# Kernel optimization log

Measured on AMD Instinct MI355X. Metric: run time of the kernel, lower is better.

Reference implementation:

```python
import jax, jax.numpy as jnp
import numpy as np

NUM_GRAPHS = 16
NODES_PER_GRAPH = 2048
FEAT_DIM = 512


def setup_inputs() -> dict:
    key = jax.random.key(0)
    batched_h = jax.random.normal(key, (NUM_GRAPHS * NODES_PER_GRAPH, FEAT_DIM), dtype=jnp.float32)
    return {
        "batched_h": batched_h,
        "num_graphs": NUM_GRAPHS,
        "nodes_per_graph": NODES_PER_GRAPH,
    }


def reference(batched_h, num_graphs, nodes_per_graph):
    # Wq = Wk = Identity (module defaults), return_feat = False.
    # Per graph g: sm[i, j] = sum_d (q[i, d] - k[j, d])^2
    # computed via the Gram-matrix identity ||q||^2 + ||k||^2 - 2 q k^T,
    # which replaces the original O(n^2 * d) tiled intermediate with a GEMM.
    h = batched_h.reshape(num_graphs, nodes_per_graph, -1)  # [G, N, D]
    q = h
    k = h
    sq_q = jnp.sum(q * q, axis=-1)                      # [G, N]
    sq_k = jnp.sum(k * k, axis=-1)                      # [G, N]
    gram = jnp.einsum("gnd,gmd->gnm", q, k)             # [G, N, N]
    sm = sq_q[:, :, None] + sq_k[:, None, :] - 2.0 * gram
    return sm  # [G, N, N] stacked analogue of the per-graph inst_out list
```

## Files before the change

### kernel.cpp

```cpp
#include <hip/hip_runtime.h>
#include <hip/hip_bf16.h>
#include <stdint.h>

#define NG 16
#define NN 2048
#define DD 512
#define NROW (NG * NN)
#define NTILE 16
#define NPAIR 136
#define NXCD 8

typedef __attribute__((ext_vector_type(8))) short short8;
typedef __attribute__((ext_vector_type(4))) float f32x4;

__device__ inline unsigned short f2bf(float f) {
  union { float f; unsigned int u; } c;
  c.f = f;
  unsigned int x = c.u;
  unsigned int r = (x + 0x7fffu + ((x >> 16) & 1u)) >> 16;
  return (unsigned short)r;
}

__device__ inline void gload_lds16(const void* g, void* l) {
  __builtin_amdgcn_global_load_lds(
      (const __attribute__((address_space(1))) void*)g,
      (__attribute__((address_space(3))) void*)l, 16, 0, 0);
}

__device__ inline void barrier_lds_only() {
  asm volatile("s_waitcnt lgkmcnt(0)" ::: "memory");
  __builtin_amdgcn_s_barrier();
}

template <bool WRITE_BF>
__global__ __launch_bounds__(256) void prep_kernel(const float* __restrict__ h,
                                                   unsigned short* __restrict__ hbf,
                                                   float* __restrict__ sq) {
  const int row = blockIdx.x * 4 + (threadIdx.x >> 6);
  const int lane = threadIdx.x & 63;
  const float* hr = h + (size_t)row * DD;
  float4 v0 = ((const float4*)hr)[lane * 2];
  float4 v1 = ((const float4*)hr)[lane * 2 + 1];
  float s = v0.x * v0.x + v0.y * v0.y + v0.z * v0.z + v0.w * v0.w +
            v1.x * v1.x + v1.y * v1.y + v1.z * v1.z + v1.w * v1.w;
  if (WRITE_BF) {
    union { unsigned short us[8]; uint4 u4; } pk;
    pk.us[0] = f2bf(v0.x); pk.us[1] = f2bf(v0.y);
    pk.us[2] = f2bf(v0.z); pk.us[3] = f2bf(v0.w);
    pk.us[4] = f2bf(v1.x); pk.us[5] = f2bf(v1.y);
    pk.us[6] = f2bf(v1.z); pk.us[7] = f2bf(v1.w);
    ((uint4*)(hbf + (size_t)row * DD))[lane] = pk.u4;
  }
#pragma unroll
  for (int off = 32; off > 0; off >>= 1) s += __shfl_xor(s, off, 64);
  if (lane == 0) sq[row] = s;
}

template <bool USE_WS>
__global__ __launch_bounds__(256) void gram_kernel(const unsigned short* __restrict__ hbf,
                                                   const float* __restrict__ hf,
                                                   const float* __restrict__ sq,
                                                   float* __restrict__ out) {
  __shared__ __align__(16) char smem[32768];
  unsigned short* As = (unsigned short*)smem;
  unsigned short* Bs = (unsigned short*)(smem + 16384);

  const int t = threadIdx.x;
  const int lane = t & 63, wid = t >> 6;
  const int wr = wid >> 1, wc = wid & 1;
  const int l16 = lane & 15, lhi = lane >> 4;

  const int bid = blockIdx.x;
  const int xcd = bid & (NXCD - 1);
  const int slot = bid >> 3;
  const int gh = (slot >= NPAIR) ? 1 : 0;
  const int g = xcd * 2 + gh;
  int p = slot - gh * NPAIR;
  int bi = 0, rowlen = NTILE;
  while (p >= rowlen) { p -= rowlen; ++bi; --rowlen; }
  const int bj = bi + p;

  {
    const int phase = (slot >> 5) & 3;
    for (int i = 0; i < phase * 3; ++i) __builtin_amdgcn_s_sleep(15);
  }

  const size_t rowA = (size_t)g * NN + bi * 128;
  const size_t rowB = (size_t)g * NN + bj * 128;

  f32x4 acc[4][4];
#pragma unroll
  for (int m = 0; m < 4; ++m)
#pragma unroll
    for (int n = 0; n < 4; ++n) acc[m][n] = (f32x4){0.f, 0.f, 0.f, 0.f};

  for (int kt = 0; kt < DD / 64; ++kt) {
    if (USE_WS) {
      const char* Ab = (const char*)(hbf + rowA * DD + kt * 64);
      const char* Bb = (const char*)(hbf + rowB * DD + kt * 64);
#pragma unroll
      for (int r = 0; r < 4; ++r) {
        const int off = r * 4096 + t * 16;
        const int rw = off >> 7;
        const int cb = off & 127;
        gload_lds16(Ab + (size_t)rw * (DD * 2) + cb, (char*)As + r * 4096 + wid * 1024);
        gload_lds16(Bb + (size_t)rw * (DD * 2) + cb, (char*)Bs + r * 4096 + wid * 1024);
      }
    } else {
      const float* Af = hf + rowA * DD + kt * 64;
      const float* Bf = hf + rowB * DD + kt * 64;
#pragma unroll
      for (int r = 0; r < 4; ++r) {
        const int off = r * 4096 + t * 16;
        const int rw = off >> 7;
        const int c0 = (off & 127) >> 1;
        float4 a0 = *(const float4*)(Af + (size_t)rw * DD + c0);
        float4 a1 = *(const float4*)(Af + (size_t)rw * DD + c0 + 4);
        float4 b0 = *(const float4*)(Bf + (size_t)rw * DD + c0);
        float4 b1 = *(const float4*)(Bf + (size_t)rw * DD + c0 + 4);
        union { unsigned short us[8]; uint4 u4; } pa, pb;
        pa.us[0] = f2bf(a0.x); pa.us[1] = f2bf(a0.y);
        pa.us[2] = f2bf(a0.z); pa.us[3] = f2bf(a0.w);
        pa.us[4] = f2bf(a1.x); pa.us[5] = f2bf(a1.y);
        pa.us[6] = f2bf(a1.z); pa.us[7] = f2bf(a1.w);
        pb.us[0] = f2bf(b0.x); pb.us[1] = f2bf(b0.y);
        pb.us[2] = f2bf(b0.z); pb.us[3] = f2bf(b0.w);
        pb.us[4] = f2bf(b1.x); pb.us[5] = f2bf(b1.y);
        pb.us[6] = f2bf(b1.z); pb.us[7] = f2bf(b1.w);
        *(uint4*)((char*)As + off) = pa.u4;
        *(uint4*)((char*)Bs + off) = pb.u4;
      }
    }
    __syncthreads();
#pragma unroll
    for (int kk = 0; kk < 2; ++kk) {
      short8 af[4], bfr[4];
#pragma unroll
      for (int m = 0; m < 4; ++m)
        af[m] = *(const short8*)&As[(wr * 64 + m * 16 + l16) * 64 + kk * 32 + lhi * 8];
#pragma unroll
      for (int n = 0; n < 4; ++n)
        bfr[n] = *(const short8*)&Bs[(wc * 64 + n * 16 + l16) * 64 + kk * 32 + lhi * 8];
#pragma unroll
      for (int m = 0; m < 4; ++m)
#pragma unroll
        for (int n = 0; n < 4; ++n)
          acc[m][n] = __builtin_amdgcn_mfma_f32_16x16x32_bf16(af[m], bfr[n], acc[m][n], 0, 0, 0);
    }
    __syncthreads();
  }

  float sqr[4][4];
  float sqc[4];
#pragma unroll
  for (int m = 0; m < 4; ++m)
#pragma unroll
    for (int r = 0; r < 4; ++r)
      sqr[m][r] = sq[rowA + wr * 64 + m * 16 + lhi * 4 + r];
#pragma unroll
  for (int n = 0; n < 4; ++n) sqc[n] = sq[rowB + wc * 64 + n * 16 + l16];

  float* outg = out + (size_t)g * NN * NN;
  const bool offdiag = (bi != bj);

#pragma unroll
  for (int hf = 0; hf < 2; ++hf) {
    if (wc == hf) {
#pragma unroll
      for (int n = 0; n < 4; ++n)
#pragma unroll
        for (int m = 0; m < 4; ++m) {
          f32x4 v;
          v.x = sqr[m][0] + sqc[n] - 2.0f * acc[m][n][0];
          v.y = sqr[m][1] + sqc[n] - 2.0f * acc[m][n][1];
          v.z = sqr[m][2] + sqc[n] - 2.0f * acc[m][n][2];
          v.w = sqr[m][3] + sqc[n] - 2.0f * acc[m][n][3];
          const int jl = n * 16 + l16;
          const int sw = (wr * 16 + m * 4 + lhi) ^ (jl & 31);
          *(f32x4*)(smem + jl * 512 + (sw << 4)) = v;
        }
    }
    barrier_lds_only();

    {
      const int jrow0 = bj * 128 + hf * 64;
      const int s = t & 31;
#pragma unroll
      for (int k = 0; k < 8; ++k) {
        const int jl = k * 8 + (t >> 5);
        f32x4 v = *(const f32x4*)(smem + jl * 512 + ((s ^ (jl & 31)) << 4));
        __builtin_nontemporal_store(
            v, (f32x4*)&outg[(size_t)(jrow0 + jl) * NN + bi * 128 + s * 4]);
      }
    }
    if (offdiag) {
      const int jcol0 = bj * 128 + hf * 64;
      const int j0 = (t & 15) * 4;
#pragma unroll
      for (int k = 0; k < 8; ++k) {
        const int ip = k * 16 + (t >> 4);
        f32x4 v;
#pragma unroll
        for (int d = 0; d < 4; ++d) {
          const int jl = j0 + d;
          v[d] = *(const float*)(smem + jl * 512 + ((((ip >> 2) ^ (jl & 31)) << 4)) +
                                 (ip & 3) * 4);
        }
        __builtin_nontemporal_store(
            v, (f32x4*)&outg[(size_t)(bi * 128 + ip) * NN + jcol0 + j0]);
      }
    }
    if (hf == 0) barrier_lds_only();
  }
}

extern "C" void kernel_launch(void* const* d_in, const int* in_sizes, int n_in,
                              void* d_out, int out_size, void* d_ws, size_t ws_size,
                              hipStream_t stream) {
  const float* h = (const float*)d_in[0];
  float* out = (float*)d_out;

  float* sq = (float*)d_ws;
  unsigned short* hbf = (unsigned short*)((char*)d_ws + NROW * 4);
  const size_t need_ws = (size_t)NROW * 4 + (size_t)NROW * DD * 2;
  const bool use_ws = ws_size >= need_ws;

  if (use_ws) {
    prep_kernel<true><<<NROW / 4, 256, 0, stream>>>(h, hbf, sq);
    gram_kernel<true><<<NG * NPAIR, 256, 0, stream>>>(hbf, nullptr, sq, out);
  } else {
    prep_kernel<false><<<NROW / 4, 256, 0, stream>>>(h, nullptr, sq);
    gram_kernel<false><<<NG * NPAIR, 256, 0, stream>>>(nullptr, h, sq, out);
  }
}
```

Before: 107.7 us.

## Enlarge symmetric Gram tiles to 256x256 with 512-thread blocks

Block tiles grow from 128x128 to 256x256 and blocks from 4 to 8 waves, so the triangular grid per graph shrinks from 136 to 36 tile pairs. Each wave now accumulates a 128x64 sub-tile. The epilogue is restructured to write the direct tile and then, for off-diagonal tiles, the transposed mirror tile through a separate XOR-swizzled LDS staging pass. The aim is to halve global/L2 operand traffic per output and cut block overhead. In exchange the grid is only 576 blocks of 64 KB LDS each, which risks poor load balance and occupancy on 256 CUs, and the epilogue needs more barriers.

Measured after the change: 122.2 us. 13.5% more time.

```diff
diff --git a/kernel.cpp b/kernel.cpp
--- a/kernel.cpp
+++ b/kernel.cpp
@@ -6,8 +6,8 @@
 #define NN 2048
 #define DD 512
 #define NROW (NG * NN)
-#define NTILE 16
-#define NPAIR 136
+#define NT8 8
+#define NPAIR8 36
 #define NXCD 8
 
 typedef __attribute__((ext_vector_type(8))) short short8;
@@ -57,40 +57,40 @@
 }
 
 template <bool USE_WS>
-__global__ __launch_bounds__(256) void gram_kernel(const unsigned short* __restrict__ hbf,
+__global__ __launch_bounds__(512) void gram_kernel(const unsigned short* __restrict__ hbf,
                                                    const float* __restrict__ hf,
                                                    const float* __restrict__ sq,
                                                    float* __restrict__ out) {
-  __shared__ __align__(16) char smem[32768];
+  __shared__ __align__(16) char smem[65536];
   unsigned short* As = (unsigned short*)smem;
-  unsigned short* Bs = (unsigned short*)(smem + 16384);
+  unsigned short* Bs = (unsigned short*)(smem + 32768);
 
   const int t = threadIdx.x;
   const int lane = t & 63, wid = t >> 6;
-  const int wr = wid >> 1, wc = wid & 1;
+  const int wr = wid >> 2, wc = wid & 3;
   const int l16 = lane & 15, lhi = lane >> 4;
 
   const int bid = blockIdx.x;
   const int xcd = bid & (NXCD - 1);
   const int slot = bid >> 3;
-  const int gh = (slot >= NPAIR) ? 1 : 0;
+  const int gh = (slot >= NPAIR8) ? 1 : 0;
   const int g = xcd * 2 + gh;
-  int p = slot - gh * NPAIR;
-  int bi = 0, rowlen = NTILE;
+  int p = slot - gh * NPAIR8;
+  int bi = 0, rowlen = NT8;
   while (p >= rowlen) { p -= rowlen; ++bi; --rowlen; }
   const int bj = bi + p;
 
   {
-    const int phase = (slot >> 5) & 3;
-    for (int i = 0; i < phase * 3; ++i) __builtin_amdgcn_s_sleep(15);
-  }
-
-  const size_t rowA = (size_t)g * NN + bi * 128;
-  const size_t rowB = (size_t)g * NN + bj * 128;
-
-  f32x4 acc[4][4];
-#pragma unroll
-  for (int m = 0; m < 4; ++m)
+    const int phase = (slot >> 5) & 1;
+    for (int i = 0; i < phase * 6; ++i) __builtin_amdgcn_s_sleep(15);
+  }
+
+  const size_t rowA = (size_t)g * NN + bi * 256;
+  const size_t rowB = (size_t)g * NN + bj * 256;
+
+  f32x4 acc[8][4];
+#pragma unroll
+  for (int m = 0; m < 8; ++m)
 #pragma unroll
     for (int n = 0; n < 4; ++n) acc[m][n] = (f32x4){0.f, 0.f, 0.f, 0.f};
 
@@ -100,18 +100,18 @@
       const char* Bb = (const char*)(hbf + rowB * DD + kt * 64);
 #pragma unroll
       for (int r = 0; r < 4; ++r) {
-        const int off = r * 4096 + t * 16;
+        const int off = r * 8192 + t * 16;
         const int rw = off >> 7;
         const int cb = off & 127;
-        gload_lds16(Ab + (size_t)rw * (DD * 2) + cb, (char*)As + r * 4096 + wid * 1024);
-        gload_lds16(Bb + (size_t)rw * (DD * 2) + cb, (char*)Bs + r * 4096 + wid * 1024);
+        gload_lds16(Ab + (size_t)rw * (DD * 2) + cb, (char*)As + r * 8192 + wid * 1024);
+        gload_lds16(Bb + (size_t)rw * (DD * 2) + cb, (char*)Bs + r * 8192 + wid * 1024);
       }
     } else {
       const float* Af = hf + rowA * DD + kt * 64;
       const float* Bf = hf + rowB * DD + kt * 64;
 #pragma unroll
       for (int r = 0; r < 4; ++r) {
-        const int off = r * 4096 + t * 16;
+        const int off = r * 8192 + t * 16;
         const int rw = off >> 7;
         const int c0 = (off & 127) >> 1;
         float4 a0 = *(const float4*)(Af + (size_t)rw * DD + c0);
@@ -134,15 +134,15 @@
     __syncthreads();
 #pragma unroll
     for (int kk = 0; kk < 2; ++kk) {
-      short8 af[4], bfr[4];
-#pragma unroll
-      for (int m = 0; m < 4; ++m)
-        af[m] = *(const short8*)&As[(wr * 64 + m * 16 + l16) * 64 + kk * 32 + lhi * 8];
+      short8 af[8], bfr[4];
+#pragma unroll
+      for (int m = 0; m < 8; ++m)
+        af[m] = *(const short8*)&As[(wr * 128 + m * 16 + l16) * 64 + kk * 32 + lhi * 8];
 #pragma unroll
       for (int n = 0; n < 4; ++n)
         bfr[n] = *(const short8*)&Bs[(wc * 64 + n * 16 + l16) * 64 + kk * 32 + lhi * 8];
 #pragma unroll
-      for (int m = 0; m < 4; ++m)
+      for (int m = 0; m < 8; ++m)
 #pragma unroll
         for (int n = 0; n < 4; ++n)
           acc[m][n] = __builtin_amdgcn_mfma_f32_16x16x32_bf16(af[m], bfr[n], acc[m][n], 0, 0, 0);
@@ -150,13 +150,13 @@
     __syncthreads();
   }
 
-  float sqr[4][4];
+  float sqr[8][4];
   float sqc[4];
 #pragma unroll
-  for (int m = 0; m < 4; ++m)
+  for (int m = 0; m < 8; ++m)
 #pragma unroll
     for (int r = 0; r < 4; ++r)
-      sqr[m][r] = sq[rowA + wr * 64 + m * 16 + lhi * 4 + r];
+      sqr[m][r] = sq[rowA + wr * 128 + m * 16 + lhi * 4 + r];
 #pragma unroll
   for (int n = 0; n < 4; ++n) sqc[n] = sq[rowB + wc * 64 + n * 16 + l16];
 
@@ -164,53 +164,72 @@
   const bool offdiag = (bi != bj);
 
 #pragma unroll
-  for (int hf = 0; hf < 2; ++hf) {
-    if (wc == hf) {
+  for (int c = 0; c < 4; ++c) {
+    if (wc == c) {
 #pragma unroll
       for (int n = 0; n < 4; ++n)
 #pragma unroll
-        for (int m = 0; m < 4; ++m) {
+        for (int m = 0; m < 8; ++m) {
           f32x4 v;
           v.x = sqr[m][0] + sqc[n] - 2.0f * acc[m][n][0];
           v.y = sqr[m][1] + sqc[n] - 2.0f * acc[m][n][1];
           v.z = sqr[m][2] + sqc[n] - 2.0f * acc[m][n][2];
           v.w = sqr[m][3] + sqc[n] - 2.0f * acc[m][n][3];
           const int jl = n * 16 + l16;
-          const int sw = (wr * 16 + m * 4 + lhi) ^ (jl & 31);
-          *(f32x4*)(smem + jl * 512 + (sw << 4)) = v;
+          const int sl = wr * 32 + m * 4 + lhi;
+          *(f32x4*)(smem + jl * 1024 + ((sl ^ (jl & 31)) << 4)) = v;
         }
     }
     barrier_lds_only();
-
     {
-      const int jrow0 = bj * 128 + hf * 64;
-      const int s = t & 31;
+      const int jrow0 = bj * 256 + c * 64;
 #pragma unroll
       for (int k = 0; k < 8; ++k) {
-        const int jl = k * 8 + (t >> 5);
-        f32x4 v = *(const f32x4*)(smem + jl * 512 + ((s ^ (jl & 31)) << 4));
+        const int idx = k * 512 + t;
+        const int jl = idx >> 6;
+        const int s = idx & 63;
+        f32x4 v = *(const f32x4*)(smem + jl * 1024 + ((s ^ (jl & 31)) << 4));
         __builtin_nontemporal_store(
-            v, (f32x4*)&outg[(size_t)(jrow0 + jl) * NN + bi * 128 + s * 4]);
-      }
-    }
-    if (offdiag) {
-      const int jcol0 = bj * 128 + hf * 64;
-      const int j0 = (t & 15) * 4;
-#pragma unroll
-      for (int k = 0; k < 8; ++k) {
-        const int ip = k * 16 + (t >> 4);
-        f32x4 v;
-#pragma unroll
-        for (int d = 0; d < 4; ++d) {
-          const int jl = j0 + d;
-          v[d] = *(const float*)(smem + jl * 512 + ((((ip >> 2) ^ (jl & 31)) << 4)) +
-                                 (ip & 3) * 4);
+            v, (f32x4*)&outg[(size_t)(jrow0 + jl) * NN + bi * 256 + s * 4]);
+      }
+    }
+    barrier_lds_only();
+  }
+
+  if (offdiag) {
+#pragma unroll
+    for (int ci = 0; ci < 4; ++ci) {
+      if (wr == (ci >> 1)) {
+#pragma unroll
+        for (int mm = 0; mm < 4; ++mm) {
+          const int m = (ci & 1) * 4 + mm;
+#pragma unroll
+          for (int n = 0; n < 4; ++n) {
+            const int jp = wc * 64 + n * 16 + l16;
+#pragma unroll
+            for (int r = 0; r < 4; ++r) {
+              const int il = mm * 16 + lhi * 4 + r;
+              const float val = sqr[m][r] + sqc[n] - 2.0f * acc[m][n][r];
+              *(float*)(smem + il * 1024 + ((jp ^ ((il & 31) << 2)) << 2)) = val;
+            }
+          }
         }
-        __builtin_nontemporal_store(
-            v, (f32x4*)&outg[(size_t)(bi * 128 + ip) * NN + jcol0 + j0]);
-      }
-    }
-    if (hf == 0) barrier_lds_only();
+      }
+      barrier_lds_only();
+      {
+        const int irow0 = bi * 256 + ci * 64;
+#pragma unroll
+        for (int k = 0; k < 8; ++k) {
+          const int idx = k * 512 + t;
+          const int il = idx >> 6;
+          const int s = idx & 63;
+          f32x4 v = *(const f32x4*)(smem + il * 1024 + ((s ^ (il & 31)) << 4));
+          __builtin_nontemporal_store(
+              v, (f32x4*)&outg[(size_t)(irow0 + il) * NN + bj * 256 + s * 4]);
+        }
+      }
+      if (ci < 3) barrier_lds_only();
+    }
   }
 }
 
@@ -227,9 +246,9 @@
 
   if (use_ws) {
     prep_kernel<true><<<NROW / 4, 256, 0, stream>>>(h, hbf, sq);
-    gram_kernel<true><<<NG * NPAIR, 256, 0, stream>>>(hbf, nullptr, sq, out);
+    gram_kernel<true><<<NG * NPAIR8, 512, 0, stream>>>(hbf, nullptr, sq, out);
   } else {
     prep_kernel<false><<<NROW / 4, 256, 0, stream>>>(h, nullptr, sq);
-    gram_kernel<false><<<NG * NPAIR, 256, 0, stream>>>(nullptr, h, sq, out);
-  }
-}
+    gram_kernel<false><<<NG * NPAIR8, 512, 0, stream>>>(nullptr, h, sq, out);
+  }
+}
```

## Halve LDS footprint with K=32 tiles and quarter-sized epilogue staging

Applied to the files above, without the earlier changes.

Shrinks the shared-memory buffer from 32KB to 16KB by loading K-slices of 32 instead of 64 per iteration, and restructures the epilogue to stage 32-row quarters. The transposed off-diagonal write becomes a separate pass that writes transposed values into LDS with scalar stores, so both global stores read full f32x4 rows. The aim is more resident blocks per CU. The cost is twice as many barrier-synchronized K iterations with less MFMA work per barrier, plus more epilogue barriers. The staggered start-sleep phase range is also widened.

After: 110.0 us. 2.1% more time.

```diff
diff --git a/kernel.cpp b/kernel.cpp
--- a/kernel.cpp
+++ b/kernel.cpp
@@ -61,9 +61,9 @@
                                                    const float* __restrict__ hf,
                                                    const float* __restrict__ sq,
                                                    float* __restrict__ out) {
-  __shared__ __align__(16) char smem[32768];
+  __shared__ __align__(16) char smem[16384];
   unsigned short* As = (unsigned short*)smem;
-  unsigned short* Bs = (unsigned short*)(smem + 16384);
+  unsigned short* Bs = (unsigned short*)(smem + 8192);
 
   const int t = threadIdx.x;
   const int lane = t & 63, wid = t >> 6;
@@ -81,7 +81,7 @@
   const int bj = bi + p;
 
   {
-    const int phase = (slot >> 5) & 3;
+    const int phase = (slot >> 5) & 7;
     for (int i = 0; i < phase * 3; ++i) __builtin_amdgcn_s_sleep(15);
   }
 
@@ -94,26 +94,26 @@
 #pragma unroll
     for (int n = 0; n < 4; ++n) acc[m][n] = (f32x4){0.f, 0.f, 0.f, 0.f};
 
-  for (int kt = 0; kt < DD / 64; ++kt) {
+  for (int kt = 0; kt < DD / 32; ++kt) {
     if (USE_WS) {
-      const char* Ab = (const char*)(hbf + rowA * DD + kt * 64);
-      const char* Bb = (const char*)(hbf + rowB * DD + kt * 64);
-#pragma unroll
-      for (int r = 0; r < 4; ++r) {
+      const char* Ab = (const char*)(hbf + rowA * DD + kt * 32);
+      const char* Bb = (const char*)(hbf + rowB * DD + kt * 32);
+#pragma unroll
+      for (int r = 0; r < 2; ++r) {
         const int off = r * 4096 + t * 16;
-        const int rw = off >> 7;
-        const int cb = off & 127;
+        const int rw = off >> 6;
+        const int cb = off & 63;
         gload_lds16(Ab + (size_t)rw * (DD * 2) + cb, (char*)As + r * 4096 + wid * 1024);
         gload_lds16(Bb + (size_t)rw * (DD * 2) + cb, (char*)Bs + r * 4096 + wid * 1024);
       }
     } else {
-      const float* Af = hf + rowA * DD + kt * 64;
-      const float* Bf = hf + rowB * DD + kt * 64;
-#pragma unroll
-      for (int r = 0; r < 4; ++r) {
+      const float* Af = hf + rowA * DD + kt * 32;
+      const float* Bf = hf + rowB * DD + kt * 32;
+#pragma unroll
+      for (int r = 0; r < 2; ++r) {
         const int off = r * 4096 + t * 16;
-        const int rw = off >> 7;
-        const int c0 = (off & 127) >> 1;
+        const int rw = off >> 6;
+        const int c0 = (off & 63) >> 1;
         float4 a0 = *(const float4*)(Af + (size_t)rw * DD + c0);
         float4 a1 = *(const float4*)(Af + (size_t)rw * DD + c0 + 4);
         float4 b0 = *(const float4*)(Bf + (size_t)rw * DD + c0);
@@ -132,15 +132,14 @@
       }
     }
     __syncthreads();
-#pragma unroll
-    for (int kk = 0; kk < 2; ++kk) {
+    {
       short8 af[4], bfr[4];
 #pragma unroll
       for (int m = 0; m < 4; ++m)
-        af[m] = *(const short8*)&As[(wr * 64 + m * 16 + l16) * 64 + kk * 32 + lhi * 8];
+        af[m] = *(const short8*)&As[(wr * 64 + m * 16 + l16) * 32 + lhi * 8];
 #pragma unroll
       for (int n = 0; n < 4; ++n)
-        bfr[n] = *(const short8*)&Bs[(wc * 64 + n * 16 + l16) * 64 + kk * 32 + lhi * 8];
+        bfr[n] = *(const short8*)&Bs[(wc * 64 + n * 16 + l16) * 32 + lhi * 8];
 #pragma unroll
       for (int m = 0; m < 4; ++m)
 #pragma unroll
@@ -164,10 +163,12 @@
   const bool offdiag = (bi != bj);
 
 #pragma unroll
-  for (int hf = 0; hf < 2; ++hf) {
-    if (wc == hf) {
-#pragma unroll
-      for (int n = 0; n < 4; ++n)
+  for (int q = 0; q < 4; ++q) {
+    if (wc == (q >> 1)) {
+#pragma unroll
+      for (int nn2 = 0; nn2 < 2; ++nn2) {
+        const int n = (q & 1) * 2 + nn2;
+        const int jrow = n * 16 + l16 - (q & 1) * 32;
 #pragma unroll
         for (int m = 0; m < 4; ++m) {
           f32x4 v;
@@ -175,42 +176,61 @@
           v.y = sqr[m][1] + sqc[n] - 2.0f * acc[m][n][1];
           v.z = sqr[m][2] + sqc[n] - 2.0f * acc[m][n][2];
           v.w = sqr[m][3] + sqc[n] - 2.0f * acc[m][n][3];
-          const int jl = n * 16 + l16;
-          const int sw = (wr * 16 + m * 4 + lhi) ^ (jl & 31);
-          *(f32x4*)(smem + jl * 512 + (sw << 4)) = v;
+          const int sl = wr * 16 + m * 4 + lhi;
+          *(f32x4*)(smem + jrow * 512 + ((sl ^ jrow) << 4)) = v;
         }
+      }
     }
     barrier_lds_only();
-
     {
-      const int jrow0 = bj * 128 + hf * 64;
-      const int s = t & 31;
-#pragma unroll
-      for (int k = 0; k < 8; ++k) {
-        const int jl = k * 8 + (t >> 5);
-        f32x4 v = *(const f32x4*)(smem + jl * 512 + ((s ^ (jl & 31)) << 4));
+      const int jrow0 = bj * 128 + q * 32;
+#pragma unroll
+      for (int k = 0; k < 4; ++k) {
+        const int idx = k * 256 + t;
+        const int jl = idx >> 5;
+        const int s = idx & 31;
+        f32x4 v = *(const f32x4*)(smem + jl * 512 + ((s ^ jl) << 4));
         __builtin_nontemporal_store(
             v, (f32x4*)&outg[(size_t)(jrow0 + jl) * NN + bi * 128 + s * 4]);
       }
     }
-    if (offdiag) {
-      const int jcol0 = bj * 128 + hf * 64;
-      const int j0 = (t & 15) * 4;
-#pragma unroll
-      for (int k = 0; k < 8; ++k) {
-        const int ip = k * 16 + (t >> 4);
-        f32x4 v;
-#pragma unroll
-        for (int d = 0; d < 4; ++d) {
-          const int jl = j0 + d;
-          v[d] = *(const float*)(smem + jl * 512 + ((((ip >> 2) ^ (jl & 31)) << 4)) +
-                                 (ip & 3) * 4);
+    barrier_lds_only();
+  }
+
+  if (offdiag) {
+#pragma unroll
+    for (int qi = 0; qi < 4; ++qi) {
+      if (wr == (qi >> 1)) {
+#pragma unroll
+        for (int mm = 0; mm < 2; ++mm) {
+          const int m = (qi & 1) * 2 + mm;
+#pragma unroll
+          for (int n = 0; n < 4; ++n) {
+            const int jp = wc * 64 + n * 16 + l16;
+#pragma unroll
+            for (int r = 0; r < 4; ++r) {
+              const int il = mm * 16 + lhi * 4 + r;
+              const float val = sqr[m][r] + sqc[n] - 2.0f * acc[m][n][r];
+              *(float*)(smem + il * 512 + (((jp >> 2) ^ il) << 4) + (jp & 3) * 4) = val;
+            }
+          }
         }
-        __builtin_nontemporal_store(
-            v, (f32x4*)&outg[(size_t)(bi * 128 + ip) * NN + jcol0 + j0]);
-      }
-    }
-    if (hf == 0) barrier_lds_only();
+      }
+      barrier_lds_only();
+      {
+        const int irow0 = bi * 128 + qi * 32;
+#pragma unroll
+        for (int k = 0; k < 4; ++k) {
+          const int idx = k * 256 + t;
+          const int il = idx >> 5;
+          const int s = idx & 31;
+          f32x4 v = *(const f32x4*)(smem + il * 512 + ((s ^ il) << 4));
+          __builtin_nontemporal_store(
+              v, (f32x4*)&outg[(size_t)(irow0 + il) * NN + bj * 128 + s * 4]);
+        }
+      }
+      if (qi < 3) barrier_lds_only();
+    }
   }
 }
 
```
